# Kernel tuning notes

Hardware: AMD Instinct MI355X
Metric: run time of the kernel (lower is better)

The kernel has to match this reference:

```python
import jax, jax.numpy as jnp
import numpy as np
import math

B, T, C = 2, 2048, 2048
H, G, HS = 16, 4, 128  # n_head, n_query_groups, head_size
EPS = 1e-5
SCALE = 1.0 / math.sqrt(HS)
QKV_DIM = (H + 2 * G) * HS  # 3072, gate logits (H) appended after


def _build_rope(seq_len, n_elem, base):
    freq = base ** (np.arange(0, n_elem, 2, dtype=np.float64) / n_elem)
    inv_freq = 1.0 / freq
    idx_theta = np.outer(np.arange(seq_len, dtype=np.float64), inv_freq)
    return (jnp.asarray(np.cos(idx_theta), dtype=jnp.float32),
            jnp.asarray(np.sin(idx_theta), dtype=jnp.float32))


def setup_inputs() -> dict:
    key = jax.random.key(0)
    k1, k2, k3 = jax.random.split(key, 3)
    x = jax.random.normal(k1, (B, T, C), dtype=jnp.float32)
    # rope base per module: 0.09 * local_window ** 1.628
    base = 0.09 * (2048.0 ** 1.628)
    cos, sin = _build_rope(T, HS, base)  # [T, HS//2]
    W_attn = jax.random.normal(k2, (QKV_DIM + H, C), dtype=jnp.float32) * 0.02
    W_proj = jax.random.normal(k3, (C, H * HS), dtype=jnp.float32) * 0.02
    q_norm_w = jnp.ones((HS,), dtype=jnp.float32)
    k_norm_w = jnp.ones((HS,), dtype=jnp.float32)
    return {"x": x, "cos": cos, "sin": sin, "W_attn": W_attn,
            "q_norm_w": q_norm_w, "k_norm_w": k_norm_w, "W_proj": W_proj}


def _rms_norm(v, w):
    # per-head RMSNorm over last dim (head_size)
    ms = jnp.mean(jnp.square(v), axis=-1, keepdims=True)
    return v * jax.lax.rsqrt(ms + EPS) * w


def _apply_rope(v, cos, sin):
    # v: [B, T, N, HS]; cos/sin: [T, HS//2]; non-interleaved halves
    d2 = v.shape[-1] // 2
    x1, x2 = v[..., :d2], v[..., d2:]
    c = cos[None, :, None, :]
    s = sin[None, :, None, :]
    return jnp.concatenate([x1 * c - x2 * s, x2 * c + x1 * s], axis=-1)


def reference(x, cos, sin, W_attn, q_norm_w, k_norm_w, W_proj):
    qkv = jnp.einsum('btc,oc->bto', x, W_attn)  # [B, T, QKV_DIM+H]
    q = qkv[..., : H * HS].reshape(B, T, H, HS)
    k = qkv[..., H * HS:(H + G) * HS].reshape(B, T, G, HS)
    v = qkv[..., (H + G) * HS: QKV_DIM].reshape(B, T, G, HS)
    gate = qkv[..., QKV_DIM:]  # [B, T, H]

    q = _apply_rope(_rms_norm(q, q_norm_w), cos, sin)
    k = _apply_rope(_rms_norm(k, k_norm_w), cos, sin)

    rep = H // G
    kr = jnp.repeat(k, rep, axis=2)  # [B, T, H, HS]
    vr = jnp.repeat(v, rep, axis=2)

    scores = jnp.einsum('bthd,bshd->bhts', q, kr) * SCALE  # [B, H, T, T]
    causal = jnp.tril(jnp.ones((T, T), dtype=bool))
    scores = jnp.where(causal, scores, jnp.finfo(scores.dtype).min)
    probs = jax.nn.softmax(scores, axis=-1)
    out = jnp.einsum('bhts,bshd->bthd', probs, vr)  # [B, T, H, HS]

    out = out * jax.nn.sigmoid(gate)[..., None]  # gated attention, per-head
    y = jnp.einsum('bto,co->btc', out.reshape(B, T, H * HS), W_proj)
    return y
```

## Files before the change

### kernel.cpp

```cpp
#include <hip/hip_runtime.h>

#define T_   2048
#define BB   2
#define CC   2048
#define HH   16
#define GG   4
#define HSS  128
#define QKVD 3072
#define NQKV 3088
#define NPAD 3200
#define SCALE_ 0.08838834764831845f

typedef __attribute__((ext_vector_type(8))) short  short8;
typedef __attribute__((ext_vector_type(4))) float  f32x4;
typedef __attribute__((ext_vector_type(4))) int    v4i;
typedef __attribute__((ext_vector_type(4))) float  v4f;
typedef __attribute__((ext_vector_type(4))) unsigned short u16x4;

typedef const void __attribute__((address_space(1)))* gas1_t;
typedef void __attribute__((address_space(3)))* as3_t;

__device__ __forceinline__ void gl_lds16(const void* g, void* l) {
    __builtin_amdgcn_global_load_lds((gas1_t)g, (as3_t)l, 16, 0, 0);
}

__device__ __forceinline__ unsigned short f2bf(float f) {
    unsigned u = __float_as_uint(f);
    u += 0x7fffu + ((u >> 16) & 1u);
    return (unsigned short)(u >> 16);
}
__device__ __forceinline__ float bf2f(unsigned short h) {
    return __uint_as_float(((unsigned)h) << 16);
}

__global__ void k_convert(const float* __restrict__ src, unsigned short* __restrict__ dst,
                          int n_src4, int n_dst4) {
    int i = blockIdx.x * blockDim.x + threadIdx.x;
    if (i >= n_dst4) return;
    u16x4 o;
    if (i < n_src4) {
        v4f v = *(const v4f*)(src + (size_t)i * 4);
        o[0] = f2bf(v[0]); o[1] = f2bf(v[1]); o[2] = f2bf(v[2]); o[3] = f2bf(v[3]);
    } else {
        o[0] = 0; o[1] = 0; o[2] = 0; o[3] = 0;
    }
    *(u16x4*)(dst + (size_t)i * 4) = o;
}

template <typename OutT>
__launch_bounds__(256, 2)
__global__ void k_gemm_nt(const unsigned short* __restrict__ A,
                          const unsigned short* __restrict__ Bm,
                          OutT* __restrict__ C,
                          int K, int lda, int ldb, int ldc) {
    __shared__ unsigned short As[128 * 64];
    __shared__ unsigned short Bs[128 * 64];
    const int t    = threadIdx.x;
    const int lane = t & 63;
    const int wid  = t >> 6;
    const int bm = blockIdx.x, bn = blockIdx.y;
    const int wm = (wid >> 1) * 64, wn = (wid & 1) * 64;

    f32x4 acc[4][4];
#pragma unroll
    for (int i = 0; i < 4; ++i)
#pragma unroll
        for (int j = 0; j < 4; ++j)
            acc[i][j] = (f32x4){0.f, 0.f, 0.f, 0.f};

    const int fro = lane & 15;
    const int fko = (lane >> 4) * 8;
    const int lrow = lane >> 3, lcol = (lane & 7) * 8;

    for (int kt = 0; kt < K; kt += 64) {
        __syncthreads();
#pragma unroll
        for (int p = 0; p < 4; ++p) {
            const int ra = wid * 32 + p * 8;
            gl_lds16(A  + (size_t)(bm * 128 + ra + lrow) * lda + kt + lcol, &As[ra * 64]);
            gl_lds16(Bm + (size_t)(bn * 128 + ra + lrow) * ldb + kt + lcol, &Bs[ra * 64]);
        }
        __syncthreads();
#pragma unroll
        for (int kk = 0; kk < 2; ++kk) {
            short8 af[4], bfr[4];
#pragma unroll
            for (int i = 0; i < 4; ++i)
                af[i] = *(const short8*)&As[(wm + i * 16 + fro) * 64 + kk * 32 + fko];
#pragma unroll
            for (int j = 0; j < 4; ++j)
                bfr[j] = *(const short8*)&Bs[(wn + j * 16 + fro) * 64 + kk * 32 + fko];
#pragma unroll
            for (int i = 0; i < 4; ++i)
#pragma unroll
                for (int j = 0; j < 4; ++j)
                    acc[i][j] = __builtin_amdgcn_mfma_f32_16x16x32_bf16(af[i], bfr[j], acc[i][j], 0, 0, 0);
        }
    }
    const int col = lane & 15, rbase = (lane >> 4) * 4;
#pragma unroll
    for (int i = 0; i < 4; ++i)
#pragma unroll
        for (int j = 0; j < 4; ++j)
#pragma unroll
            for (int r = 0; r < 4; ++r) {
                int grow = bm * 128 + wm + i * 16 + rbase + r;
                int gcol = bn * 128 + wn + j * 16 + col;
                float v = acc[i][j][r];
                if constexpr (sizeof(OutT) == 2)
                    C[(size_t)grow * ldc + gcol] = (OutT)f2bf(v);
                else
                    C[(size_t)grow * ldc + gcol] = (OutT)v;
            }
}

__global__ void k_normrope(unsigned short* __restrict__ qkv,
                           const float* __restrict__ cosT, const float* __restrict__ sinT,
                           const float* __restrict__ qw, const float* __restrict__ kw) {
    const int lane = threadIdx.x & 63;
    const int row  = blockIdx.x * 4 + (threadIdx.x >> 6);
    const int tok  = row / 20;
    const int hh   = row - tok * 20;
    const int tpos = tok & (T_ - 1);
    unsigned short* rp = qkv + (size_t)tok * NPAD + (hh < 16 ? hh * 128 : 2048 + (hh - 16) * 128);
    const float* w = (hh < 16) ? qw : kw;
    float e1 = bf2f(rp[lane]);
    float e2 = bf2f(rp[lane + 64]);
    float ss = e1 * e1 + e2 * e2;
#pragma unroll
    for (int m = 1; m < 64; m <<= 1) ss += __shfl_xor(ss, m);
    float inv = rsqrtf(ss * (1.0f / 128.0f) + 1e-5f);
    float n1 = e1 * inv * w[lane];
    float n2 = e2 * inv * w[lane + 64];
    float c = cosT[tpos * 64 + lane];
    float s = sinT[tpos * 64 + lane];
    rp[lane]      = f2bf(n1 * c - n2 * s);
    rp[lane + 64] = f2bf(n2 * c + n1 * s);
}

__global__ void k_transposeV(const unsigned short* __restrict__ qkv,
                             unsigned short* __restrict__ vt) {
    __shared__ unsigned short tile[64][65];
    const int b = blockIdx.x >> 2, g = blockIdx.x & 3;
    const int s0 = blockIdx.y * 64, d0 = blockIdx.z * 64;
    const int tx = threadIdx.x & 63, ty0 = threadIdx.x >> 6;
    const unsigned short* src = qkv + (size_t)(b * T_ + s0) * NPAD + 2560 + g * 128 + d0;
#pragma unroll
    for (int r = 0; r < 16; ++r) {
        int ty = ty0 * 16 + r;
        tile[ty][tx] = src[(size_t)ty * NPAD + tx];
    }
    __syncthreads();
    unsigned short* dstp = vt + ((size_t)(b * GG + g) * 128 + d0) * T_ + s0;
#pragma unroll
    for (int r = 0; r < 16; ++r) {
        int ty = ty0 * 16 + r;
        dstp[(size_t)ty * T_ + tx] = tile[tx][ty];
    }
}

__launch_bounds__(256, 2)
__global__ void k_attn(const unsigned short* __restrict__ qkv,
                       const unsigned short* __restrict__ vt,
                       unsigned short* __restrict__ ao) {
    __shared__ unsigned short Ks[2][64 * 128];
    __shared__ unsigned short Vs[2][128 * 64];
    __shared__ unsigned short Ps[4][16 * 72];
    const int t = threadIdx.x;
    const int lane = t & 63;
    const int wid  = t >> 6;
    const int id = blockIdx.x;
    const int bg = id & 7;
    const int hh = (id >> 3) & 3;
    const int pr = id >> 5;
    const int b = bg >> 2, g = bg & 3, h = g * 4 + hh;
    const int fro = lane & 15, fk = lane >> 4;
    const int rbase = fk * 4;

    const unsigned short* kg0 = qkv + (size_t)(b * T_) * NPAD + 2048 + g * 128;
    const unsigned short* vg0 = vt + (size_t)(b * GG + g) * 128 * T_;

    const int cp0 = wid * 4;
    int cur = 0;

#pragma unroll
    for (int seg = 0; seg < 2; ++seg) {
        const int qt = (seg == 0) ? pr : 31 - pr;
        const int q0w = qt * 64 + wid * 16;

        short8 qf[4];
        const unsigned short* qp = qkv + (size_t)(b * T_ + q0w + fro) * NPAD + h * 128 + fk * 8;
#pragma unroll
        for (int kb = 0; kb < 4; ++kb) qf[kb] = *(const short8*)(qp + kb * 32);

        float m_r[4], l_r[4];
        f32x4 o[8];
#pragma unroll
        for (int r = 0; r < 4; ++r) { m_r[r] = -1e30f; l_r[r] = 0.f; }
#pragma unroll
        for (int d = 0; d < 8; ++d) o[d] = (f32x4){0.f, 0.f, 0.f, 0.f};

        const int nt = qt + 1;

#pragma unroll
        for (int p = 0; p < 4; ++p) {
            const int cp = cp0 + p;
            const int kr = cp * 4 + (lane >> 4);
            const int sK = lane & 15;
            gl_lds16(kg0 + (size_t)(0 + kr) * NPAD + (size_t)((sK ^ (kr & 7)) * 8), &Ks[cur][cp * 512]);
            const int d  = cp * 8 + (lane >> 3);
            const int sV = lane & 7;
            gl_lds16(vg0 + (size_t)d * T_ + 0 + (size_t)((sV ^ (d & 7)) * 8), &Vs[cur][cp * 512]);
        }
        __syncthreads();

        for (int ti = 0; ti < nt; ++ti) {
            if (ti + 1 < nt) {
                const int sn = (ti + 1) * 64;
#pragma unroll
                for (int p = 0; p < 4; ++p) {
                    const int cp = cp0 + p;
                    const int kr = cp * 4 + (lane >> 4);
                    const int sK = lane & 15;
                    gl_lds16(kg0 + (size_t)(sn + kr) * NPAD + (size_t)((sK ^ (kr & 7)) * 8), &Ks[cur ^ 1][cp * 512]);
                    const int d  = cp * 8 + (lane >> 3);
                    const int sV = lane & 7;
                    gl_lds16(vg0 + (size_t)d * T_ + sn + (size_t)((sV ^ (d & 7)) * 8), &Vs[cur ^ 1][cp * 512]);
                }
            }
            f32x4 sc[4];
#pragma unroll
            for (int jb = 0; jb < 4; ++jb) sc[jb] = (f32x4){0.f, 0.f, 0.f, 0.f};
#pragma unroll
            for (int jb = 0; jb < 4; ++jb) {
                const int kr = jb * 16 + fro;
#pragma unroll
                for (int kb = 0; kb < 4; ++kb) {
                    short8 kf = *(const short8*)&Ks[cur][kr * 128 + 8 * ((kb * 4 + fk) ^ (kr & 7))];
                    sc[jb] = __builtin_amdgcn_mfma_f32_16x16x32_bf16(qf[kb], kf, sc[jb], 0, 0, 0);
                }
            }
            const bool domask = (ti == qt);
#pragma unroll
            for (int jb = 0; jb < 4; ++jb)
#pragma unroll
                for (int r = 0; r < 4; ++r) {
                    float v = sc[jb][r] * SCALE_;
                    if (domask && (jb * 16 + fro) > (wid * 16 + rbase + r)) v = -1e30f;
                    sc[jb][r] = v;
                }
            float mx[4], fs[4], rs[4];
#pragma unroll
            for (int r = 0; r < 4; ++r)
                mx[r] = fmaxf(fmaxf(sc[0][r], sc[1][r]), fmaxf(sc[2][r], sc[3][r]));
#pragma unroll
            for (int msk = 1; msk < 16; msk <<= 1)
#pragma unroll
                for (int r = 0; r < 4; ++r) mx[r] = fmaxf(mx[r], __shfl_xor(mx[r], msk));
#pragma unroll
            for (int r = 0; r < 4; ++r) {
                float mn = fmaxf(m_r[r], mx[r]);
                fs[r] = __expf(m_r[r] - mn);
                m_r[r] = mn;
            }
#pragma unroll
            for (int jb = 0; jb < 4; ++jb)
#pragma unroll
                for (int r = 0; r < 4; ++r) sc[jb][r] = __expf(sc[jb][r] - m_r[r]);
#pragma unroll
            for (int r = 0; r < 4; ++r)
                rs[r] = (sc[0][r] + sc[1][r]) + (sc[2][r] + sc[3][r]);
#pragma unroll
            for (int msk = 1; msk < 16; msk <<= 1)
#pragma unroll
                for (int r = 0; r < 4; ++r) rs[r] += __shfl_xor(rs[r], msk);
#pragma unroll
            for (int r = 0; r < 4; ++r) l_r[r] = l_r[r] * fs[r] + rs[r];
#pragma unroll
            for (int d = 0; d < 8; ++d)
#pragma unroll
                for (int r = 0; r < 4; ++r) o[d][r] *= fs[r];
            unsigned short* pw = &Ps[wid][0];
#pragma unroll
            for (int jb = 0; jb < 4; ++jb)
#pragma unroll
                for (int r = 0; r < 4; ++r)
                    pw[(rbase + r) * 72 + jb * 16 + fro] = f2bf(sc[jb][r]);
            asm volatile("s_waitcnt lgkmcnt(0)" ::: "memory");
            __builtin_amdgcn_sched_barrier(0);
            short8 pa[2];
#pragma unroll
            for (int ks = 0; ks < 2; ++ks)
                pa[ks] = *(const short8*)&Ps[wid][fro * 72 + ks * 32 + fk * 8];
#pragma unroll
            for (int ks = 0; ks < 2; ++ks)
#pragma unroll
                for (int db = 0; db < 8; ++db) {
                    const int d = db * 16 + fro;
                    short8 vf = *(const short8*)&Vs[cur][d * 64 + 8 * ((ks * 4 + fk) ^ (d & 7))];
                    o[db] = __builtin_amdgcn_mfma_f32_16x16x32_bf16(pa[ks], vf, o[db], 0, 0, 0);
                }
            __syncthreads();
            cur ^= 1;
        }
#pragma unroll
        for (int r = 0; r < 4; ++r) {
            const int qrow = q0w + rbase + r;
            float gv = bf2f(qkv[(size_t)(b * T_ + qrow) * NPAD + QKVD + h]);
            float sg = 1.f / (1.f + __expf(-gv));
            float invl = sg / l_r[r];
            unsigned short* orow = ao + (size_t)(b * T_ + qrow) * 2048 + h * 128;
#pragma unroll
            for (int db = 0; db < 8; ++db)
                orow[db * 16 + fro] = f2bf(o[db][r] * invl);
        }
    }
}

extern "C" void kernel_launch(void* const* d_in, const int* in_sizes, int n_in,
                              void* d_out, int out_size, void* d_ws, size_t ws_size,
                              hipStream_t stream) {
    const float* x      = (const float*)d_in[0];
    const float* cosT   = (const float*)d_in[1];
    const float* sinT   = (const float*)d_in[2];
    const float* W_attn = (const float*)d_in[3];
    const float* qw     = (const float*)d_in[4];
    const float* kw     = (const float*)d_in[5];
    const float* W_proj = (const float*)d_in[6];

    char* ws = (char*)d_ws;
    const size_t OFF_XB   = 0;
    const size_t OFF_WAB  = 16777216;
    const size_t OFF_WPB  = 29884416;
    const size_t OFF_QKV  = 38273024;
    const size_t OFF_VT   = 64487424;
    const size_t OFF_AO   = 68681728;
    const size_t NEED     = 85458944;
    if (ws_size < NEED) return;

    unsigned short* xb   = (unsigned short*)(ws + OFF_XB);
    unsigned short* wab  = (unsigned short*)(ws + OFF_WAB);
    unsigned short* wpb  = (unsigned short*)(ws + OFF_WPB);
    unsigned short* qkvb = (unsigned short*)(ws + OFF_QKV);
    unsigned short* vtb  = (unsigned short*)(ws + OFF_VT);
    unsigned short* aob  = (unsigned short*)(ws + OFF_AO);

    k_convert<<<8192, 256, 0, stream>>>(x,      xb,  2097152, 2097152);
    k_convert<<<6400, 256, 0, stream>>>(W_attn, wab, 1581056, 1638400);
    k_convert<<<4096, 256, 0, stream>>>(W_proj, wpb, 1048576, 1048576);
    k_gemm_nt<unsigned short><<<dim3(32, 25), 256, 0, stream>>>(xb, wab, qkvb, 2048, 2048, 2048, NPAD);
    k_normrope<<<20480, 256, 0, stream>>>(qkvb, cosT, sinT, qw, kw);
    k_transposeV<<<dim3(8, 32, 2), 256, 0, stream>>>(qkvb, vtb);
    k_attn<<<512, 256, 0, stream>>>(qkvb, vtb, aob);
    k_gemm_nt<float><<<dim3(32, 16), 256, 0, stream>>>(aob, wpb, (float*)d_out, 2048, 2048, 2048, 2048);
}
```

Baseline: 259.3 us.

## Add explicit vmcnt waits, lazy softmax rescale, exp2 scaling, and MFMA priority

Replaces __syncthreads with a partial vmcnt wait plus s_barrier, so the next K/V tile prefetch can remain in flight while the current tile is processed. Folds log2(e) into the scale and uses exp2f. Rescales the running max and output accumulators only when some row's max grows by more than 8 (a lazy-rescale trick). Raises wave priority around the MFMA blocks and pads the P buffer stride to 76 to change the LDS bank mapping. The lazy rescale relies on fp32 headroom, and the hand-written vmcnt counts must match the number of outstanding loads for correctness.

```diff
diff --git a/kernel.cpp b/kernel.cpp
--- a/kernel.cpp
+++ b/kernel.cpp
@@ -10,6 +10,7 @@
 #define NQKV 3088
 #define NPAD 3200
 #define SCALE_ 0.08838834764831845f
+#define SCALE2_ (0.08838834764831845f * 1.4426950408889634f)
 
 typedef __attribute__((ext_vector_type(8))) short  short8;
 typedef __attribute__((ext_vector_type(4))) float  f32x4;
@@ -165,7 +166,7 @@
                        unsigned short* __restrict__ ao) {
     __shared__ unsigned short Ks[2][64 * 128];
     __shared__ unsigned short Vs[2][128 * 64];
-    __shared__ unsigned short Ps[4][16 * 72];
+    __shared__ unsigned short Ps[4][16 * 76];
     const int t = threadIdx.x;
     const int lane = t & 63;
     const int wid  = t >> 6;
@@ -207,12 +208,11 @@
             const int cp = cp0 + p;
             const int kr = cp * 4 + (lane >> 4);
             const int sK = lane & 15;
-            gl_lds16(kg0 + (size_t)(0 + kr) * NPAD + (size_t)((sK ^ (kr & 7)) * 8), &Ks[cur][cp * 512]);
+            gl_lds16(kg0 + (size_t)kr * NPAD + (size_t)((sK ^ (kr & 7)) * 8), &Ks[cur][cp * 512]);
             const int d  = cp * 8 + (lane >> 3);
             const int sV = lane & 7;
-            gl_lds16(vg0 + (size_t)d * T_ + 0 + (size_t)((sV ^ (d & 7)) * 8), &Vs[cur][cp * 512]);
-        }
-        __syncthreads();
+            gl_lds16(vg0 + (size_t)d * T_ + (size_t)((sV ^ (d & 7)) * 8), &Vs[cur][cp * 512]);
+        }
 
         for (int ti = 0; ti < nt; ++ti) {
             if (ti + 1 < nt) {
@@ -227,10 +227,17 @@
                     const int sV = lane & 7;
                     gl_lds16(vg0 + (size_t)d * T_ + sn + (size_t)((sV ^ (d & 7)) * 8), &Vs[cur ^ 1][cp * 512]);
                 }
+                asm volatile("s_waitcnt vmcnt(8)" ::: "memory");
+            } else {
+                asm volatile("s_waitcnt vmcnt(0)" ::: "memory");
             }
+            __builtin_amdgcn_s_barrier();
+            __builtin_amdgcn_sched_barrier(0);
+
             f32x4 sc[4];
 #pragma unroll
             for (int jb = 0; jb < 4; ++jb) sc[jb] = (f32x4){0.f, 0.f, 0.f, 0.f};
+            __builtin_amdgcn_s_setprio(1);
 #pragma unroll
             for (int jb = 0; jb < 4; ++jb) {
                 const int kr = jb * 16 + fro;
@@ -240,16 +247,17 @@
                     sc[jb] = __builtin_amdgcn_mfma_f32_16x16x32_bf16(qf[kb], kf, sc[jb], 0, 0, 0);
                 }
             }
+            __builtin_amdgcn_s_setprio(0);
             const bool domask = (ti == qt);
 #pragma unroll
             for (int jb = 0; jb < 4; ++jb)
 #pragma unroll
                 for (int r = 0; r < 4; ++r) {
-                    float v = sc[jb][r] * SCALE_;
+                    float v = sc[jb][r] * SCALE2_;
                     if (domask && (jb * 16 + fro) > (wid * 16 + rbase + r)) v = -1e30f;
                     sc[jb][r] = v;
                 }
-            float mx[4], fs[4], rs[4];
+            float mx[4], rs[4];
 #pragma unroll
             for (int r = 0; r < 4; ++r)
                 mx[r] = fmaxf(fmaxf(sc[0][r], sc[1][r]), fmaxf(sc[2][r], sc[3][r]));
@@ -257,16 +265,24 @@
             for (int msk = 1; msk < 16; msk <<= 1)
 #pragma unroll
                 for (int r = 0; r < 4; ++r) mx[r] = fmaxf(mx[r], __shfl_xor(mx[r], msk));
-#pragma unroll
-            for (int r = 0; r < 4; ++r) {
-                float mn = fmaxf(m_r[r], mx[r]);
-                fs[r] = __expf(m_r[r] - mn);
-                m_r[r] = mn;
+            bool grow = false;
+#pragma unroll
+            for (int r = 0; r < 4; ++r) grow = grow || (mx[r] > m_r[r] + 8.f);
+            if (__any(grow ? 1 : 0)) {
+#pragma unroll
+                for (int r = 0; r < 4; ++r) {
+                    float mn = fmaxf(m_r[r], mx[r]);
+                    float fs = exp2f(m_r[r] - mn);
+                    m_r[r] = mn;
+                    l_r[r] *= fs;
+#pragma unroll
+                    for (int d = 0; d < 8; ++d) o[d][r] *= fs;
+                }
             }
 #pragma unroll
             for (int jb = 0; jb < 4; ++jb)
 #pragma unroll
-                for (int r = 0; r < 4; ++r) sc[jb][r] = __expf(sc[jb][r] - m_r[r]);
+                for (int r = 0; r < 4; ++r) sc[jb][r] = exp2f(sc[jb][r] - m_r[r]);
 #pragma unroll
             for (int r = 0; r < 4; ++r)
                 rs[r] = (sc[0][r] + sc[1][r]) + (sc[2][r] + sc[3][r]);
@@ -275,23 +291,20 @@
 #pragma unroll
                 for (int r = 0; r < 4; ++r) rs[r] += __shfl_xor(rs[r], msk);
 #pragma unroll
-            for (int r = 0; r < 4; ++r) l_r[r] = l_r[r] * fs[r] + rs[r];
-#pragma unroll
-            for (int d = 0; d < 8; ++d)
-#pragma unroll
-                for (int r = 0; r < 4; ++r) o[d][r] *= fs[r];
+            for (int r = 0; r < 4; ++r) l_r[r] += rs[r];
             unsigned short* pw = &Ps[wid][0];
 #pragma unroll
             for (int jb = 0; jb < 4; ++jb)
 #pragma unroll
                 for (int r = 0; r < 4; ++r)
-                    pw[(rbase + r) * 72 + jb * 16 + fro] = f2bf(sc[jb][r]);
+                    pw[(rbase + r) * 76 + jb * 16 + fro] = f2bf(sc[jb][r]);
             asm volatile("s_waitcnt lgkmcnt(0)" ::: "memory");
             __builtin_amdgcn_sched_barrier(0);
             short8 pa[2];
 #pragma unroll
             for (int ks = 0; ks < 2; ++ks)
-                pa[ks] = *(const short8*)&Ps[wid][fro * 72 + ks * 32 + fk * 8];
+                pa[ks] = *(const short8*)&Ps[wid][fro * 76 + ks * 32 + fk * 8];
+            __builtin_amdgcn_s_setprio(1);
 #pragma unroll
             for (int ks = 0; ks < 2; ++ks)
 #pragma unroll
@@ -300,7 +313,8 @@
                     short8 vf = *(const short8*)&Vs[cur][d * 64 + 8 * ((ks * 4 + fk) ^ (d & 7))];
                     o[db] = __builtin_amdgcn_mfma_f32_16x16x32_bf16(pa[ks], vf, o[db], 0, 0, 0);
                 }
-            __syncthreads();
+            __builtin_amdgcn_s_setprio(0);
+            __builtin_amdgcn_s_barrier();
             cur ^= 1;
         }
 #pragma unroll
```

Measured after the change: 266.6 us. 1.03x slower.

## Replace GEMM with 256x256-tile double-buffered swizzled 8-wave kernel

Applied to the files above, without the earlier changes.

Both projection GEMMs now use a new kernel with 256x256 output tiles, 512 threads (8 waves), and double-buffered LDS with an XOR-swizzled layout. The next K-slice is prefetched in chunks spread between MFMA groups, and MFMA bursts run at raised wave priority. The aim is more reuse per loaded byte, hidden global-load latency and fewer LDS bank conflicts. The trade-off is far fewer blocks (208 and 128) on a GPU with many CUs, about 128KB of LDS per block, and B-tile reads past the padded weight rows whose results are dropped by a column bound.

```diff
diff --git a/kernel.cpp b/kernel.cpp
--- a/kernel.cpp
+++ b/kernel.cpp
@@ -48,70 +48,116 @@
 }
 
 template <typename OutT>
-__launch_bounds__(256, 2)
-__global__ void k_gemm_nt(const unsigned short* __restrict__ A,
-                          const unsigned short* __restrict__ Bm,
-                          OutT* __restrict__ C,
-                          int K, int lda, int ldb, int ldc) {
-    __shared__ unsigned short As[128 * 64];
-    __shared__ unsigned short Bs[128 * 64];
-    const int t    = threadIdx.x;
+__launch_bounds__(512, 2)
+__global__ void k_gemm8(const unsigned short* __restrict__ A,
+                        const unsigned short* __restrict__ Bm,
+                        OutT* __restrict__ C,
+                        int K, int lda, int ldb, int ldc, int nmax) {
+    __shared__ unsigned short As[2][256 * 64];
+    __shared__ unsigned short Bs[2][256 * 64];
+    const int t = threadIdx.x;
     const int lane = t & 63;
     const int wid  = t >> 6;
+    const int wr = wid >> 2, wc = wid & 3;
     const int bm = blockIdx.x, bn = blockIdx.y;
-    const int wm = (wid >> 1) * 64, wn = (wid & 1) * 64;
-
-    f32x4 acc[4][4];
-#pragma unroll
-    for (int i = 0; i < 4; ++i)
-#pragma unroll
-        for (int j = 0; j < 4; ++j)
-            acc[i][j] = (f32x4){0.f, 0.f, 0.f, 0.f};
-
-    const int fro = lane & 15;
-    const int fko = (lane >> 4) * 8;
-    const int lrow = lane >> 3, lcol = (lane & 7) * 8;
-
+    const int fro = lane & 15, fk = lane >> 4;
+
+    const int srow  = lane >> 3;
+    const size_t scol = (size_t)(((lane & 7) ^ srow) * 8);
+
+    const unsigned short* Abase = A  + (size_t)(bm * 256) * lda;
+    const unsigned short* Bbase = Bm + (size_t)(bn * 256) * ldb;
+
+    f32x4 acc[8][4];
+#pragma unroll
+    for (int i = 0; i < 8; ++i)
+#pragma unroll
+        for (int j = 0; j < 4; ++j) acc[i][j] = (f32x4){0.f, 0.f, 0.f, 0.f};
+
+#pragma unroll
+    for (int h = 0; h < 2; ++h)
+#pragma unroll
+        for (int c8 = 0; c8 < 2; ++c8) {
+            const int rr = h * 128 + wid * 16 + c8 * 8;
+            gl_lds16(Abase + (size_t)(rr + srow) * lda + scol, &As[0][rr * 64]);
+            gl_lds16(Bbase + (size_t)(rr + srow) * ldb + scol, &Bs[0][rr * 64]);
+        }
+
+    int cur = 0;
     for (int kt = 0; kt < K; kt += 64) {
-        __syncthreads();
-#pragma unroll
-        for (int p = 0; p < 4; ++p) {
-            const int ra = wid * 32 + p * 8;
-            gl_lds16(A  + (size_t)(bm * 128 + ra + lrow) * lda + kt + lcol, &As[ra * 64]);
-            gl_lds16(Bm + (size_t)(bn * 128 + ra + lrow) * ldb + kt + lcol, &Bs[ra * 64]);
-        }
-        __syncthreads();
-#pragma unroll
-        for (int kk = 0; kk < 2; ++kk) {
-            short8 af[4], bfr[4];
-#pragma unroll
-            for (int i = 0; i < 4; ++i)
-                af[i] = *(const short8*)&As[(wm + i * 16 + fro) * 64 + kk * 32 + fko];
-#pragma unroll
-            for (int j = 0; j < 4; ++j)
-                bfr[j] = *(const short8*)&Bs[(wn + j * 16 + fro) * 64 + kk * 32 + fko];
-#pragma unroll
-            for (int i = 0; i < 4; ++i)
-#pragma unroll
-                for (int j = 0; j < 4; ++j)
-                    acc[i][j] = __builtin_amdgcn_mfma_f32_16x16x32_bf16(af[i], bfr[j], acc[i][j], 0, 0, 0);
-        }
+        asm volatile("s_waitcnt vmcnt(0)" ::: "memory");
+        __builtin_amdgcn_s_barrier();
+        __builtin_amdgcn_sched_barrier(0);
+        const bool pf = (kt + 64 < K);
+        const int nxt = cur ^ 1;
+        const int kn = kt + 64;
+
+        short8 bf_[4][2];
+#pragma unroll
+        for (int q = 0; q < 4; ++q) {
+            short8 af[2][2];
+#pragma unroll
+            for (int im = 0; im < 2; ++im)
+#pragma unroll
+                for (int kk = 0; kk < 2; ++kk) {
+                    const int ar = wr * 128 + (q * 2 + im) * 16 + fro;
+                    af[im][kk] = *(const short8*)&As[cur][ar * 64 + ((kk * 4 + fk) ^ (ar & 7)) * 8];
+                }
+            if (q == 0) {
+#pragma unroll
+                for (int ni = 0; ni < 4; ++ni)
+#pragma unroll
+                    for (int kk = 0; kk < 2; ++kk) {
+                        const int br = wc * 64 + ni * 16 + fro;
+                        bf_[ni][kk] = *(const short8*)&Bs[cur][br * 64 + ((kk * 4 + fk) ^ (br & 7)) * 8];
+                    }
+            }
+            if (pf) {
+                const int h = q & 1;
+#pragma unroll
+                for (int c8 = 0; c8 < 2; ++c8) {
+                    const int rr = h * 128 + wid * 16 + c8 * 8;
+                    if ((q >> 1) == 0)
+                        gl_lds16(Abase + (size_t)(rr + srow) * lda + kn + scol, &As[nxt][rr * 64]);
+                    else
+                        gl_lds16(Bbase + (size_t)(rr + srow) * ldb + kn + scol, &Bs[nxt][rr * 64]);
+                }
+            }
+            __builtin_amdgcn_s_setprio(1);
+#pragma unroll
+            for (int im = 0; im < 2; ++im)
+#pragma unroll
+                for (int ni = 0; ni < 4; ++ni)
+#pragma unroll
+                    for (int kk = 0; kk < 2; ++kk)
+                        acc[q * 2 + im][ni] = __builtin_amdgcn_mfma_f32_16x16x32_bf16(
+                            af[im][kk], bf_[ni][kk], acc[q * 2 + im][ni], 0, 0, 0);
+            __builtin_amdgcn_s_setprio(0);
+            __builtin_amdgcn_s_barrier();
+        }
+        cur ^= 1;
     }
-    const int col = lane & 15, rbase = (lane >> 4) * 4;
-#pragma unroll
-    for (int i = 0; i < 4; ++i)
-#pragma unroll
-        for (int j = 0; j < 4; ++j)
-#pragma unroll
-            for (int r = 0; r < 4; ++r) {
-                int grow = bm * 128 + wm + i * 16 + rbase + r;
-                int gcol = bn * 128 + wn + j * 16 + col;
-                float v = acc[i][j][r];
-                if constexpr (sizeof(OutT) == 2)
-                    C[(size_t)grow * ldc + gcol] = (OutT)f2bf(v);
-                else
-                    C[(size_t)grow * ldc + gcol] = (OutT)v;
-            }
+
+    const int col16 = lane & 15, rbase = (lane >> 4) * 4;
+    const int gr0 = bm * 256 + wr * 128;
+    const int gc0 = bn * 256 + wc * 64;
+#pragma unroll
+    for (int mi = 0; mi < 8; ++mi)
+#pragma unroll
+        for (int ni = 0; ni < 4; ++ni) {
+            const int gcol = gc0 + ni * 16 + col16;
+            if (gcol < nmax) {
+#pragma unroll
+                for (int r = 0; r < 4; ++r) {
+                    const int grow = gr0 + mi * 16 + rbase + r;
+                    float v = acc[mi][ni][r];
+                    if constexpr (sizeof(OutT) == 2)
+                        C[(size_t)grow * ldc + gcol] = (OutT)f2bf(v);
+                    else
+                        C[(size_t)grow * ldc + gcol] = (OutT)v;
+                }
+            }
+        }
 }
 
 __global__ void k_normrope(unsigned short* __restrict__ qkv,
@@ -207,10 +253,10 @@
             const int cp = cp0 + p;
             const int kr = cp * 4 + (lane >> 4);
             const int sK = lane & 15;
-            gl_lds16(kg0 + (size_t)(0 + kr) * NPAD + (size_t)((sK ^ (kr & 7)) * 8), &Ks[cur][cp * 512]);
+            gl_lds16(kg0 + (size_t)kr * NPAD + (size_t)((sK ^ (kr & 7)) * 8), &Ks[cur][cp * 512]);
             const int d  = cp * 8 + (lane >> 3);
             const int sV = lane & 7;
-            gl_lds16(vg0 + (size_t)d * T_ + 0 + (size_t)((sV ^ (d & 7)) * 8), &Vs[cur][cp * 512]);
+            gl_lds16(vg0 + (size_t)d * T_ + (size_t)((sV ^ (d & 7)) * 8), &Vs[cur][cp * 512]);
         }
         __syncthreads();
 
@@ -348,9 +394,9 @@
     k_convert<<<8192, 256, 0, stream>>>(x,      xb,  2097152, 2097152);
     k_convert<<<6400, 256, 0, stream>>>(W_attn, wab, 1581056, 1638400);
     k_convert<<<4096, 256, 0, stream>>>(W_proj, wpb, 1048576, 1048576);
-    k_gemm_nt<unsigned short><<<dim3(32, 25), 256, 0, stream>>>(xb, wab, qkvb, 2048, 2048, 2048, NPAD);
+    k_gemm8<unsigned short><<<dim3(16, 13), 512, 0, stream>>>(xb, wab, qkvb, 2048, 2048, 2048, NPAD, NPAD);
     k_normrope<<<20480, 256, 0, stream>>>(qkvb, cosT, sinT, qw, kw);
     k_transposeV<<<dim3(8, 32, 2), 256, 0, stream>>>(qkvb, vtb);
     k_attn<<<512, 256, 0, stream>>>(qkvb, vtb, aob);
-    k_gemm_nt<float><<<dim3(32, 16), 256, 0, stream>>>(aob, wpb, (float*)d_out, 2048, 2048, 2048, 2048);
-}
+    k_gemm8<float><<<dim3(16, 8), 512, 0, stream>>>(aob, wpb, (float*)d_out, 2048, 2048, 2048, 2048, 2048);
+}
```

Result: faster. 246.3 us (-5.0%).
